# Optimization experiments

Measured on AMD Instinct MI355X. Metric: run time of the kernel, lower is better.

The kernel has to match this reference:

```python
import jax, jax.numpy as jnp
import numpy as np

MESH_RESOLUTION = 0.1
ORDER = 3  # TSC interpolation


def setup_inputs() -> dict:
    key = jax.random.key(0)
    k1, k2 = jax.random.split(key)
    L = 20.0
    N, C = 100000, 8
    positions = jax.random.uniform(k1, (N, 3), dtype=jnp.float32) * L
    cell = jnp.eye(3, dtype=jnp.float32) * L
    embeddings = jax.random.normal(k2, (N, C), dtype=jnp.float32)
    return {"positions": positions, "cell": cell, "embeddings": embeddings}


def _weights_order3(dist):
    # dist: [N,3]; returns [3,N,3]
    d2 = dist * dist
    return jnp.stack([
        0.125 * (1.0 - 4.0 * dist + 4.0 * d2),
        0.25 * (3.0 - 4.0 * d2),
        0.125 * (1.0 + 4.0 * dist + 4.0 * d2),
    ])


def reference(positions, cell, embeddings):
    # Mesh setup (cubic box)
    mesh_size = float(jnp.trace(cell)) / 3.0
    n_mesh = int(2 * round(mesh_size / (2.0 * MESH_RESOLUTION)))
    spacing = mesh_size / n_mesh
    C = embeddings.shape[1]

    positions_cell = positions / spacing  # [N,3]
    # odd order: nearest-grid-point centering
    idx = jnp.round(positions_cell).astype(jnp.int32)  # [N,3]
    dist = positions_cell - idx.astype(positions_cell.dtype)  # [N,3]

    w = _weights_order3(dist)  # [3,N,3]
    offs = jnp.arange(1 - (ORDER + 1) // 2, 1 + ORDER // 2)  # [-1,0,1]
    rp = (idx[None, :, :] + offs[:, None, None]) % n_mesh  # [3,N,3]

    xs, ys, zs = jnp.meshgrid(jnp.arange(ORDER), jnp.arange(ORDER), jnp.arange(ORDER), indexing='ij')
    xs, ys, zs = xs.ravel(), ys.ravel(), zs.ravel()  # [27]

    # flat grid indices and combined weights per (corner, atom)
    flat_idx = (rp[xs, :, 0] * n_mesh + rp[ys, :, 1]) * n_mesh + rp[zs, :, 2]  # [27,N]
    wprod = w[xs, :, 0] * w[ys, :, 1] * w[zs, :, 2]  # [27,N]

    vals = wprod[:, :, None] * embeddings[None, :, :]  # [27,N,C]
    grid = jnp.zeros((n_mesh ** 3, C), dtype=positions.dtype)
    grid = grid.at[flat_idx.reshape(-1)].add(vals.reshape(-1, C))
    # -> (C, n, n, n) to match mesh.values layout
    return grid.reshape(n_mesh, n_mesh, n_mesh, C).transpose(3, 0, 1, 2)
```

## Files before the change

### kernel.cpp

```cpp
#include <hip/hip_runtime.h>
#include <math.h>


#define KColCAP 16
#define TYS 2
#define BLK 128

typedef float nfloat4 __attribute__((ext_vector_type(4)));

__device__ __forceinline__ float tsc_w(int o, float d) {
    float t = 0.5f + (float)o * d;
    return (o == 0) ? (0.75f - d * d) : (0.5f * t * t);
}

__device__ __forceinline__ float inv_spacing(const float* __restrict__ cell, int n) {
    float tr = cell[0] + cell[4] + cell[8];
    return (3.0f * (float)n) / tr;
}


__global__ __launch_bounds__(256) void fill_recs(
    const float* __restrict__ pos, const float* __restrict__ cell,
    const float* __restrict__ emb,
    int* __restrict__ counts, int* __restrict__ ovf_cnt,
    float4* __restrict__ binrec, int* __restrict__ ovf,
    int N, int n)
{
    int i = blockIdx.x * blockDim.x + threadIdx.x;
    if (i >= N) return;
    float inv_sp = inv_spacing(cell, n);
    float px = pos[3 * i + 0] * inv_sp;
    float py = pos[3 * i + 1] * inv_sp;
    float pz = pos[3 * i + 2] * inv_sp;
    int cx = (int)rintf(px); if (cx >= n) cx -= n; else if (cx < 0) cx += n;
    int cy = (int)rintf(py); if (cy >= n) cy -= n; else if (cy < 0) cy += n;
    int bin = cx * n + cy;
    int slot = atomicAdd(&counts[bin], 1);
    if (slot < KColCAP) {
        const float4* e4 = (const float4*)(emb + (size_t)i * 8);
        float4* r = binrec + (size_t)(bin * KColCAP + slot) * 3;
        r[0] = make_float4(px, py, pz, 0.0f);
        r[1] = e4[0];
        r[2] = e4[1];
    } else {
        int o = atomicAdd(ovf_cnt, 1);
        ovf[o] = i;
    }
}


__global__ __launch_bounds__(BLK) void deposit_slab2(
    const float4* __restrict__ binrec, const int* __restrict__ counts,
    float* __restrict__ out, int n, int nyg)
{
    extern __shared__ float lds[];
    const int tid = threadIdx.x;
    const int b = blockIdx.x;
    const int x = b / nyg, yg = b - x * nyg;
    const int y0 = yg * TYS;
    const int plane = TYS * n;
    const int sz4 = (8 * plane) >> 2;

    for (int i = tid; i < sz4; i += BLK)
        ((float4*)lds)[i] = make_float4(0.f, 0.f, 0.f, 0.f);

    __shared__ int s_base[12], s_cnt[12], s_pref[13];
    if (tid < 12) {
        int dxb = tid / 4 - 1;
        int jy  = tid & 3;
        int xb = x + dxb; if (xb < 0) xb += n; else if (xb >= n) xb -= n;
        int yb = y0 - 1 + jy; if (yb < 0) yb += n; else if (yb >= n) yb -= n;
        int bin = xb * n + yb;
        s_base[tid] = bin * KColCAP;
        int c = counts[bin];
        s_cnt[tid] = (c < KColCAP) ? c : KColCAP;
    }
    __syncthreads();
    if (tid == 0) {
        int r = 0;
        #pragma unroll
        for (int j = 0; j < 12; ++j) { s_pref[j] = r; r += s_cnt[j]; }
        s_pref[12] = r;
    }
    __syncthreads();
    const int tot = s_pref[12];
    const int half = n >> 1;

    for (int v = tid; v < tot; v += BLK) {
        int j = 0;
        #pragma unroll
        for (int k = 1; k < 12; ++k) j += (v >= s_pref[k]);
        const float4* rp = binrec + (size_t)(s_base[j] + (v - s_pref[j])) * 3;
        float4 P  = rp[0];
        float4 e0 = rp[1];
        float4 e1 = rp[2];

        int cx = (int)rintf(P.x); float dx = P.x - (float)cx;
        int cy = (int)rintf(P.y); float dy = P.y - (float)cy;
        int cz = (int)rintf(P.z); float dz = P.z - (float)cz;
        if (cx >= n) cx -= n; else if (cx < 0) cx += n;
        if (cy >= n) cy -= n; else if (cy < 0) cy += n;
        if (cz >= n) cz -= n; else if (cz < 0) cz += n;

        int rx = cx - x;  if (rx > half) rx -= n; else if (rx < -half) rx += n;
        int ry = cy - y0; if (ry > half) ry -= n; else if (ry < -half) ry += n;

        float wx = tsc_w(-rx, dx);

        float wys[3] = { wx * tsc_w(-1, dy), wx * tsc_w(0, dy), wx * tsc_w(1, dy) };
        float wzs[3] = { tsc_w(-1, dz), tsc_w(0, dz), tsc_w(1, dz) };
        int lz0 = cz - 1; if (lz0 < 0) lz0 += n;
        int lz2 = cz + 1; if (lz2 >= n) lz2 -= n;
        int lzs[3] = { lz0, cz, lz2 };

        #pragma unroll
        for (int kb = 0; kb < 3; ++kb) {
            int ly = ry + kb - 1;
            if (ly < 0 || ly >= TYS) continue;
            float wvy = wys[kb];
            #pragma unroll
            for (int kc = 0; kc < 3; ++kc) {
                float w = wvy * wzs[kc];
                float* p = lds + ly * n + lzs[kc];
                atomicAdd(p + 0 * plane, w * e0.x);
                atomicAdd(p + 1 * plane, w * e0.y);
                atomicAdd(p + 2 * plane, w * e0.z);
                atomicAdd(p + 3 * plane, w * e0.w);
                atomicAdd(p + 4 * plane, w * e1.x);
                atomicAdd(p + 5 * plane, w * e1.y);
                atomicAdd(p + 6 * plane, w * e1.z);
                atomicAdd(p + 7 * plane, w * e1.w);
            }
        }
    }
    __syncthreads();

    const size_t n3 = (size_t)n * n * n;
    const int chunk = plane >> 2;
    #pragma unroll
    for (int ch = 0; ch < 8; ++ch) {
        const nfloat4* src = (const nfloat4*)(lds + (size_t)ch * plane);
        nfloat4* dst = (nfloat4*)(out + (size_t)ch * n3 + (size_t)x * n * n + (size_t)y0 * n);
        for (int i = tid; i < chunk; i += BLK)
            __builtin_nontemporal_store(src[i], dst + i);
    }
}

__global__ __launch_bounds__(256) void deposit_overflow(
    const float* __restrict__ pos, const float* __restrict__ cell,
    const float* __restrict__ emb, const int* __restrict__ ovf_cnt,
    const int* __restrict__ ovf, float* __restrict__ out, int n)
{
    int m = *ovf_cnt;
    int i = blockIdx.x * blockDim.x + threadIdx.x;
    if (i >= m) return;
    int ai = ovf[i];
    float inv_sp = inv_spacing(cell, n);
    float p[3], d[3]; int c0[3];
    #pragma unroll
    for (int kk = 0; kk < 3; ++kk) {
        p[kk] = pos[3 * ai + kk] * inv_sp;
        c0[kk] = (int)rintf(p[kk]);
        d[kk] = p[kk] - (float)c0[kk];
    }
    float w[3][3];
    #pragma unroll
    for (int kk = 0; kk < 3; ++kk) {
        float dd = d[kk];
        w[kk][0] = tsc_w(-1, dd); w[kk][1] = tsc_w(0, dd); w[kk][2] = tsc_w(1, dd);
    }
    int W[3][3];
    #pragma unroll
    for (int kk = 0; kk < 3; ++kk)
        #pragma unroll
        for (int a = 0; a < 3; ++a) {
            int v = c0[kk] - 1 + a; if (v < 0) v += n; else if (v >= n) v -= n;
            W[kk][a] = v;
        }
    size_t n3 = (size_t)n * n * n;
    const float4* e4 = (const float4*)(emb + (size_t)ai * 8);
    float4 e0 = e4[0], e1 = e4[1];
    float e[8] = {e0.x, e0.y, e0.z, e0.w, e1.x, e1.y, e1.z, e1.w};
    for (int a = 0; a < 3; ++a)
        for (int bq = 0; bq < 3; ++bq)
            for (int cq = 0; cq < 3; ++cq) {
                float wt = w[0][a] * w[1][bq] * w[2][cq];
                size_t g = ((size_t)W[0][a] * n + W[1][bq]) * n + W[2][cq];
                #pragma unroll
                for (int ch = 0; ch < 8; ++ch)
                    atomicAdd(out + (size_t)ch * n3 + g, wt * e[ch]);
            }
}


__global__ __launch_bounds__(256) void deposit_tsc8_ilv(
    const float* __restrict__ pos,
    const float* __restrict__ cell,
    const float* __restrict__ emb,
    float* __restrict__ ws,
    int total, int n)
{
    int t = blockIdx.x * blockDim.x + threadIdx.x;
    if (t >= total) return;
    int atom = t / 27;
    int c    = t - atom * 27;
    int a    = c / 9;
    int rem  = c - a * 9;
    int b    = rem / 3;
    int cc   = rem - b * 3;

    float inv_sp = inv_spacing(cell, n);

    float px = pos[3 * atom + 0] * inv_sp;
    float py = pos[3 * atom + 1] * inv_sp;
    float pz = pos[3 * atom + 2] * inv_sp;

    int cx = (int)rintf(px);  float dx = px - (float)cx;
    int cy = (int)rintf(py);  float dy = py - (float)cy;
    int cz = (int)rintf(pz);  float dz = pz - (float)cz;

    float w = tsc_w(a - 1, dx) * tsc_w(b - 1, dy) * tsc_w(cc - 1, dz);

    int x = cx - 1 + a;  if (x < 0) x += n; else if (x >= n) x -= n;
    int y = cy - 1 + b;  if (y < 0) y += n; else if (y >= n) y -= n;
    int z = cz - 1 + cc; if (z < 0) z += n; else if (z >= n) z -= n;

    const float4* e4 = (const float4*)(emb + (size_t)atom * 8);
    float4 e0 = e4[0], e1 = e4[1];

    float* p = ws + ((size_t)((x * n + y) * n + z)) * 8;
    atomicAdd(p + 0, w * e0.x);
    atomicAdd(p + 1, w * e0.y);
    atomicAdd(p + 2, w * e0.z);
    atomicAdd(p + 3, w * e0.w);
    atomicAdd(p + 4, w * e1.x);
    atomicAdd(p + 5, w * e1.y);
    atomicAdd(p + 6, w * e1.z);
    atomicAdd(p + 7, w * e1.w);
}

__global__ __launch_bounds__(256) void transpose_ilv8(
    const float* __restrict__ ws, float* __restrict__ out, int n3)
{
    int t = blockIdx.x * blockDim.x + threadIdx.x;
    int g0 = t * 4;
    if (g0 >= n3) return;
    const float4* w4 = (const float4*)(ws + (size_t)g0 * 8);
    float4 r0 = w4[0], r1 = w4[1];
    float4 r2 = w4[2], r3 = w4[3];
    float4 r4 = w4[4], r5 = w4[5];
    float4 r6 = w4[6], r7 = w4[7];

    *(float4*)(out + (size_t)0 * n3 + g0) = make_float4(r0.x, r2.x, r4.x, r6.x);
    *(float4*)(out + (size_t)1 * n3 + g0) = make_float4(r0.y, r2.y, r4.y, r6.y);
    *(float4*)(out + (size_t)2 * n3 + g0) = make_float4(r0.z, r2.z, r4.z, r6.z);
    *(float4*)(out + (size_t)3 * n3 + g0) = make_float4(r0.w, r2.w, r4.w, r6.w);
    *(float4*)(out + (size_t)4 * n3 + g0) = make_float4(r1.x, r3.x, r5.x, r7.x);
    *(float4*)(out + (size_t)5 * n3 + g0) = make_float4(r1.y, r3.y, r5.y, r7.y);
    *(float4*)(out + (size_t)6 * n3 + g0) = make_float4(r1.z, r3.z, r5.z, r7.z);
    *(float4*)(out + (size_t)7 * n3 + g0) = make_float4(r1.w, r3.w, r5.w, r7.w);
}


__global__ __launch_bounds__(256) void deposit_tsc_gen(
    const float* __restrict__ pos,
    const float* __restrict__ cell,
    const float* __restrict__ emb,
    float* __restrict__ out,
    int N, int n, int C)
{
    int i = blockIdx.x * blockDim.x + threadIdx.x;
    if (i >= N) return;

    float inv_sp = inv_spacing(cell, n);

    float p[3], d[3];
    int c0[3];
    #pragma unroll
    for (int k = 0; k < 3; ++k) {
        p[k] = pos[3 * i + k] * inv_sp;
        c0[k] = (int)rintf(p[k]);
        d[k] = p[k] - (float)c0[k];
    }
    float w[3][3];
    #pragma unroll
    for (int k = 0; k < 3; ++k) {
        float dd = d[k], d2 = dd * dd;
        w[k][0] = 0.125f * (1.0f - 4.0f * dd + 4.0f * d2);
        w[k][1] = 0.25f  * (3.0f - 4.0f * d2);
        w[k][2] = 0.125f * (1.0f + 4.0f * dd + 4.0f * d2);
    }
    int W[3][3];
    #pragma unroll
    for (int k = 0; k < 3; ++k) {
        #pragma unroll
        for (int a = 0; a < 3; ++a) {
            int v = c0[k] - 1 + a; if (v < 0) v += n; else if (v >= n) v -= n;
            W[k][a] = v;
        }
    }
    int n3 = n * n * n;
    for (int a = 0; a < 3; ++a)
        for (int b = 0; b < 3; ++b)
            for (int cc = 0; cc < 3; ++cc) {
                float wt = w[0][a] * w[1][b] * w[2][cc];
                int g = (W[0][a] * n + W[1][b]) * n + W[2][cc];
                for (int ch = 0; ch < C; ++ch)
                    atomicAdd(out + (size_t)ch * n3 + g, wt * emb[(size_t)i * C + ch]);
            }
}

extern "C" void kernel_launch(void* const* d_in, const int* in_sizes, int n_in,
                              void* d_out, int out_size, void* d_ws, size_t ws_size,
                              hipStream_t stream) {
    const float* pos  = (const float*)d_in[0];
    const float* cell = (const float*)d_in[1];
    const float* emb  = (const float*)d_in[2];
    float* out = (float*)d_out;
    float* ws  = (float*)d_ws;

    int N = in_sizes[0] / 3;
    int C = in_sizes[2] / N;
    long long n3l = (long long)out_size / C;
    int n = (int)llroundf(cbrtf((float)n3l));
    int n3 = (int)n3l;

    int block = 256;

    {
        int nb = n * n;
        size_t lds_bytes = (size_t)8 * TYS * n * sizeof(float);
        size_t rec_off = (((size_t)nb + 4 + (size_t)N) * sizeof(int) + 15) & ~(size_t)15;
        size_t need = rec_off + (size_t)nb * KColCAP * 48;
        bool slab_ok = (C == 8) && (n % TYS == 0) && n >= 8 && n <= 512
                       && lds_bytes <= 64 * 1024
                       && ws_size >= need
                       && ((long long)n * n * n == n3l);
        if (slab_ok) {
            int* counts  = (int*)d_ws;
            int* ovf_cnt = counts + nb;
            int* ovf     = counts + nb + 4;
            float4* binrec = (float4*)((char*)d_ws + rec_off);

            (void)hipMemsetAsync(counts, 0, (size_t)(nb + 4) * sizeof(int), stream);
            fill_recs<<<(N + block - 1) / block, block, 0, stream>>>(
                pos, cell, emb, counts, ovf_cnt, binrec, ovf, N, n);
            int nyg = n / TYS;
            deposit_slab2<<<n * nyg, BLK, lds_bytes, stream>>>(
                binrec, counts, out, n, nyg);
            deposit_overflow<<<(N + block - 1) / block, block, 0, stream>>>(
                pos, cell, emb, ovf_cnt, ovf, out, n);
            return;
        }
    }

    size_t need = (size_t)out_size * sizeof(float);
    if (C == 8 && ws_size >= need && (n3 % 4) == 0) {
        (void)hipMemsetAsync(d_ws, 0, need, stream);
        int total = N * 27;
        deposit_tsc8_ilv<<<(total + block - 1) / block, block, 0, stream>>>(
            pos, cell, emb, ws, total, n);
        int tthreads = n3 / 4;
        transpose_ilv8<<<(tthreads + block - 1) / block, block, 0, stream>>>(
            ws, out, n3);
    } else {
        (void)hipMemsetAsync(d_out, 0, (size_t)out_size * sizeof(float), stream);
        int grid = (N + block - 1) / block;
        deposit_tsc_gen<<<grid, block, 0, stream>>>(pos, cell, emb, out, N, n, C);
    }
}
```

Measured before the change: 157.9 us.

## Convert slab deposit kernel into persistent blocks looping over contiguous tiles

Replaces the one-block-per-(x, y-pair) slab deposit launch with a persistent kernel of about 2048 blocks. Each block processes a contiguous range of tiles, zeroing LDS, gathering and accumulating bin records, then streaming the tile out with a flattened channel-major store loop. The aim is to cut block launch and scheduling overhead across the 20000 small tiles and to improve locality in the per-block bin reads. In exchange each block now runs its tiles serially with an extra barrier per tile, and load balance can get worse. The slab path's size limit also tightens to n at most 256.

```diff
diff --git a/kernel.cpp b/kernel.cpp
--- a/kernel.cpp
+++ b/kernel.cpp
@@ -5,6 +5,7 @@
 #define KColCAP 16
 #define TYS 2
 #define BLK 128
+#define BPCU 8
 
 typedef float nfloat4 __attribute__((ext_vector_type(4)));
 
@@ -49,100 +50,108 @@
 }
 
 
-__global__ __launch_bounds__(BLK) void deposit_slab2(
+__global__ __launch_bounds__(BLK) void deposit_persist(
     const float4* __restrict__ binrec, const int* __restrict__ counts,
-    float* __restrict__ out, int n, int nyg)
+    float* __restrict__ out, int n, int nyg, int ntiles, int tpb)
 {
     extern __shared__ float lds[];
     const int tid = threadIdx.x;
-    const int b = blockIdx.x;
-    const int x = b / nyg, yg = b - x * nyg;
-    const int y0 = yg * TYS;
     const int plane = TYS * n;
-    const int sz4 = (8 * plane) >> 2;
-
-    for (int i = tid; i < sz4; i += BLK)
-        ((float4*)lds)[i] = make_float4(0.f, 0.f, 0.f, 0.f);
+    const int q4 = plane >> 2;
+    const int nf4 = 8 * q4;
+    const int half = n >> 1;
+    const size_t n3 = (size_t)n * n * n;
 
     __shared__ int s_base[12], s_cnt[12], s_pref[13];
-    if (tid < 12) {
-        int dxb = tid / 4 - 1;
-        int jy  = tid & 3;
-        int xb = x + dxb; if (xb < 0) xb += n; else if (xb >= n) xb -= n;
-        int yb = y0 - 1 + jy; if (yb < 0) yb += n; else if (yb >= n) yb -= n;
-        int bin = xb * n + yb;
-        s_base[tid] = bin * KColCAP;
-        int c = counts[bin];
-        s_cnt[tid] = (c < KColCAP) ? c : KColCAP;
-    }
-    __syncthreads();
-    if (tid == 0) {
-        int r = 0;
-        #pragma unroll
-        for (int j = 0; j < 12; ++j) { s_pref[j] = r; r += s_cnt[j]; }
-        s_pref[12] = r;
-    }
-    __syncthreads();
-    const int tot = s_pref[12];
-    const int half = n >> 1;
-
-    for (int v = tid; v < tot; v += BLK) {
-        int j = 0;
-        #pragma unroll
-        for (int k = 1; k < 12; ++k) j += (v >= s_pref[k]);
-        const float4* rp = binrec + (size_t)(s_base[j] + (v - s_pref[j])) * 3;
-        float4 P  = rp[0];
-        float4 e0 = rp[1];
-        float4 e1 = rp[2];
-
-        int cx = (int)rintf(P.x); float dx = P.x - (float)cx;
-        int cy = (int)rintf(P.y); float dy = P.y - (float)cy;
-        int cz = (int)rintf(P.z); float dz = P.z - (float)cz;
-        if (cx >= n) cx -= n; else if (cx < 0) cx += n;
-        if (cy >= n) cy -= n; else if (cy < 0) cy += n;
-        if (cz >= n) cz -= n; else if (cz < 0) cz += n;
-
-        int rx = cx - x;  if (rx > half) rx -= n; else if (rx < -half) rx += n;
-        int ry = cy - y0; if (ry > half) ry -= n; else if (ry < -half) ry += n;
-
-        float wx = tsc_w(-rx, dx);
-
-        float wys[3] = { wx * tsc_w(-1, dy), wx * tsc_w(0, dy), wx * tsc_w(1, dy) };
-        float wzs[3] = { tsc_w(-1, dz), tsc_w(0, dz), tsc_w(1, dz) };
-        int lz0 = cz - 1; if (lz0 < 0) lz0 += n;
-        int lz2 = cz + 1; if (lz2 >= n) lz2 -= n;
-        int lzs[3] = { lz0, cz, lz2 };
-
-        #pragma unroll
-        for (int kb = 0; kb < 3; ++kb) {
-            int ly = ry + kb - 1;
-            if (ly < 0 || ly >= TYS) continue;
-            float wvy = wys[kb];
+
+    int t0 = blockIdx.x * tpb;
+    int t1 = t0 + tpb; if (t1 > ntiles) t1 = ntiles;
+
+    for (int t = t0; t < t1; ++t) {
+        const int x = t / nyg, yg = t - x * nyg;
+        const int y0 = yg * TYS;
+
+        for (int i = tid; i < nf4; i += BLK)
+            ((nfloat4*)lds)[i] = (nfloat4)(0.f);
+
+        if (tid < 12) {
+            int dxb = tid / 4 - 1;
+            int jy  = tid & 3;
+            int xb = x + dxb; if (xb < 0) xb += n; else if (xb >= n) xb -= n;
+            int yb = y0 - 1 + jy; if (yb < 0) yb += n; else if (yb >= n) yb -= n;
+            int bin = xb * n + yb;
+            s_base[tid] = bin * KColCAP;
+            int c = counts[bin];
+            s_cnt[tid] = (c < KColCAP) ? c : KColCAP;
+        }
+        __syncthreads();
+        if (tid == 0) {
+            int r = 0;
             #pragma unroll
-            for (int kc = 0; kc < 3; ++kc) {
-                float w = wvy * wzs[kc];
-                float* p = lds + ly * n + lzs[kc];
-                atomicAdd(p + 0 * plane, w * e0.x);
-                atomicAdd(p + 1 * plane, w * e0.y);
-                atomicAdd(p + 2 * plane, w * e0.z);
-                atomicAdd(p + 3 * plane, w * e0.w);
-                atomicAdd(p + 4 * plane, w * e1.x);
-                atomicAdd(p + 5 * plane, w * e1.y);
-                atomicAdd(p + 6 * plane, w * e1.z);
-                atomicAdd(p + 7 * plane, w * e1.w);
+            for (int j = 0; j < 12; ++j) { s_pref[j] = r; r += s_cnt[j]; }
+            s_pref[12] = r;
+        }
+        __syncthreads();
+        const int tot = s_pref[12];
+
+        for (int v = tid; v < tot; v += BLK) {
+            int j = 0;
+            #pragma unroll
+            for (int k = 1; k < 12; ++k) j += (v >= s_pref[k]);
+            const float4* rp = binrec + (size_t)(s_base[j] + (v - s_pref[j])) * 3;
+            float4 P  = rp[0];
+            float4 e0 = rp[1];
+            float4 e1 = rp[2];
+
+            int cx = (int)rintf(P.x); float dx = P.x - (float)cx;
+            int cy = (int)rintf(P.y); float dy = P.y - (float)cy;
+            int cz = (int)rintf(P.z); float dz = P.z - (float)cz;
+            if (cx >= n) cx -= n; else if (cx < 0) cx += n;
+            if (cy >= n) cy -= n; else if (cy < 0) cy += n;
+            if (cz >= n) cz -= n; else if (cz < 0) cz += n;
+
+            int rx = cx - x;  if (rx > half) rx -= n; else if (rx < -half) rx += n;
+            int ry = cy - y0; if (ry > half) ry -= n; else if (ry < -half) ry += n;
+
+            float wx = tsc_w(-rx, dx);
+
+            float wys[3] = { wx * tsc_w(-1, dy), wx * tsc_w(0, dy), wx * tsc_w(1, dy) };
+            float wzs[3] = { tsc_w(-1, dz), tsc_w(0, dz), tsc_w(1, dz) };
+            int lz0 = cz - 1; if (lz0 < 0) lz0 += n;
+            int lz2 = cz + 1; if (lz2 >= n) lz2 -= n;
+            int lzs[3] = { lz0, cz, lz2 };
+
+            #pragma unroll
+            for (int kb = 0; kb < 3; ++kb) {
+                int ly = ry + kb - 1;
+                if (ly < 0 || ly >= TYS) continue;
+                float wvy = wys[kb];
+                #pragma unroll
+                for (int kc = 0; kc < 3; ++kc) {
+                    float w = wvy * wzs[kc];
+                    float* p = lds + ly * n + lzs[kc];
+                    atomicAdd(p + 0 * plane, w * e0.x);
+                    atomicAdd(p + 1 * plane, w * e0.y);
+                    atomicAdd(p + 2 * plane, w * e0.z);
+                    atomicAdd(p + 3 * plane, w * e0.w);
+                    atomicAdd(p + 4 * plane, w * e1.x);
+                    atomicAdd(p + 5 * plane, w * e1.y);
+                    atomicAdd(p + 6 * plane, w * e1.z);
+                    atomicAdd(p + 7 * plane, w * e1.w);
+                }
             }
         }
-    }
-    __syncthreads();
-
-    const size_t n3 = (size_t)n * n * n;
-    const int chunk = plane >> 2;
-    #pragma unroll
-    for (int ch = 0; ch < 8; ++ch) {
-        const nfloat4* src = (const nfloat4*)(lds + (size_t)ch * plane);
-        nfloat4* dst = (nfloat4*)(out + (size_t)ch * n3 + (size_t)x * n * n + (size_t)y0 * n);
-        for (int i = tid; i < chunk; i += BLK)
-            __builtin_nontemporal_store(src[i], dst + i);
+        __syncthreads();
+
+        float* outb = out + (size_t)x * n * n + (size_t)y0 * n;
+        for (int i = tid; i < nf4; i += BLK) {
+            int ch = i / q4;
+            int q  = i - ch * q4;
+            nfloat4 v = ((const nfloat4*)lds)[i];
+            __builtin_nontemporal_store(
+                v, (nfloat4*)(outb + (size_t)ch * n3) + q);
+        }
+        __syncthreads();
     }
 }
 
@@ -332,7 +341,7 @@
         size_t lds_bytes = (size_t)8 * TYS * n * sizeof(float);
         size_t rec_off = (((size_t)nb + 4 + (size_t)N) * sizeof(int) + 15) & ~(size_t)15;
         size_t need = rec_off + (size_t)nb * KColCAP * 48;
-        bool slab_ok = (C == 8) && (n % TYS == 0) && n >= 8 && n <= 512
+        bool slab_ok = (C == 8) && (n % TYS == 0) && n >= 8 && n <= 256
                        && lds_bytes <= 64 * 1024
                        && ws_size >= need
                        && ((long long)n * n * n == n3l);
@@ -345,9 +354,15 @@
             (void)hipMemsetAsync(counts, 0, (size_t)(nb + 4) * sizeof(int), stream);
             fill_recs<<<(N + block - 1) / block, block, 0, stream>>>(
                 pos, cell, emb, counts, ovf_cnt, binrec, ovf, N, n);
+
             int nyg = n / TYS;
-            deposit_slab2<<<n * nyg, BLK, lds_bytes, stream>>>(
-                binrec, counts, out, n, nyg);
+            int ntiles = n * nyg;
+            int nblocks = 256 * BPCU;
+            if (nblocks > ntiles) nblocks = ntiles;
+            int tpb = (ntiles + nblocks - 1) / nblocks;
+            deposit_persist<<<nblocks, BLK, lds_bytes, stream>>>(
+                binrec, counts, out, n, nyg, ntiles, tpb);
+
             deposit_overflow<<<(N + block - 1) / block, block, 0, stream>>>(
                 pos, cell, emb, ovf_cnt, ovf, out, n);
             return;
```

New measurement: 179.2 us. 1.13x slower.

## Persistent producer-consumer deposit kernel with double-buffered LDS slabs

Applied to the files above, without the earlier changes.

Replaces the one-block-per-tile slab deposit with a persistent kernel over a fixed grid of blocks. In each block, half the threads scatter particles into one LDS buffer with atomics while the other half stream the previous tile's buffer to global memory. The aim is to overlap the global writeback with the LDS accumulation and to amortise block launch and zeroing. It also pads the channel stride, uses a custom LDS barrier, and computes the prefix sums in registers. In exchange, only 128 threads accumulate per tile, LDS use doubles, and the path is now limited to n <= 256.

```diff
diff --git a/kernel.cpp b/kernel.cpp
--- a/kernel.cpp
+++ b/kernel.cpp
@@ -4,9 +4,17 @@
 
 #define KColCAP 16
 #define TYS 2
-#define BLK 128
+#define BLK 256
+#define NBLK 1536
 
 typedef float nfloat4 __attribute__((ext_vector_type(4)));
+
+__device__ __forceinline__ void block_sync_lds() {
+    __builtin_amdgcn_sched_barrier(0);
+    asm volatile("s_waitcnt lgkmcnt(0)" ::: "memory");
+    __builtin_amdgcn_s_barrier();
+    __builtin_amdgcn_sched_barrier(0);
+}
 
 __device__ __forceinline__ float tsc_w(int o, float d) {
     float t = 0.5f + (float)o * d;
@@ -49,100 +57,138 @@
 }
 
 
-__global__ __launch_bounds__(BLK) void deposit_slab2(
+__global__ __launch_bounds__(BLK) void deposit_pc(
     const float4* __restrict__ binrec, const int* __restrict__ counts,
-    float* __restrict__ out, int n, int nyg)
+    float* __restrict__ out, int n, int nyg, int ntiles)
 {
     extern __shared__ float lds[];
     const int tid = threadIdx.x;
-    const int b = blockIdx.x;
-    const int x = b / nyg, yg = b - x * nyg;
-    const int y0 = yg * TYS;
+    const int bid = blockIdx.x;
+    const int grid = gridDim.x;
     const int plane = TYS * n;
-    const int sz4 = (8 * plane) >> 2;
-
-    for (int i = tid; i < sz4; i += BLK)
-        ((float4*)lds)[i] = make_float4(0.f, 0.f, 0.f, 0.f);
-
-    __shared__ int s_base[12], s_cnt[12], s_pref[13];
-    if (tid < 12) {
-        int dxb = tid / 4 - 1;
-        int jy  = tid & 3;
-        int xb = x + dxb; if (xb < 0) xb += n; else if (xb >= n) xb -= n;
-        int yb = y0 - 1 + jy; if (yb < 0) yb += n; else if (yb >= n) yb -= n;
-        int bin = xb * n + yb;
-        s_base[tid] = bin * KColCAP;
-        int c = counts[bin];
-        s_cnt[tid] = (c < KColCAP) ? c : KColCAP;
-    }
-    __syncthreads();
-    if (tid == 0) {
-        int r = 0;
+    const int cstr = plane + 4;
+    const int bufsz = 8 * cstr;
+    const int q4 = plane >> 2;
+    const int half = n >> 1;
+    const size_t n3 = (size_t)n * n * n;
+    const bool producer = (tid < 128);
+    const int ctid = tid - 128;
+
+    int iter = 0;
+    int pt = -1;
+
+    for (int t = bid; t < ntiles; t += grid, ++iter) {
+        const int p = iter & 1;
+        float* bufp = lds + p * bufsz;
+
+        if (producer) {
+            nfloat4* z4 = (nfloat4*)bufp;
+            const int nz4 = bufsz >> 2;
+            for (int i = tid; i < nz4; i += 128)
+                z4[i] = (nfloat4)(0.f);
+        } else if (iter > 0) {
+            const float* src = lds + (p ^ 1) * bufsz;
+            const int px_ = pt / nyg, pyg = pt - px_ * nyg;
+            const int py0 = pyg * TYS;
+            float* outb = out + (size_t)px_ * n * n + (size_t)py0 * n;
+            #pragma unroll
+            for (int ch = 0; ch < 8; ++ch) {
+                const nfloat4* s4 = (const nfloat4*)(src + ch * cstr);
+                nfloat4* d4 = (nfloat4*)(outb + (size_t)ch * n3);
+                for (int q = ctid; q < q4; q += 128)
+                    __builtin_nontemporal_store(s4[q], d4 + q);
+            }
+        }
+        block_sync_lds();
+
+        if (producer) {
+            const int x = t / nyg, yg = t - x * nyg;
+            const int y0 = yg * TYS;
+
+            int base[12], pref[13];
+            pref[0] = 0;
+            #pragma unroll
+            for (int j = 0; j < 12; ++j) {
+                int dxb = j >> 2;
+                int jy  = j & 3;
+                int xb = x + dxb - 1; if (xb < 0) xb += n; else if (xb >= n) xb -= n;
+                int yb = y0 - 1 + jy; if (yb < 0) yb += n; else if (yb >= n) yb -= n;
+                int bin = xb * n + yb;
+                base[j] = bin * KColCAP;
+                int c = counts[bin];
+                c = (c < KColCAP) ? c : KColCAP;
+                pref[j + 1] = pref[j] + c;
+            }
+            const int tot = pref[12];
+
+            for (int v = tid; v < tot; v += 128) {
+                int rec = base[0] + v;
+                #pragma unroll
+                for (int k = 1; k < 12; ++k) {
+                    int cand = base[k] + (v - pref[k]);
+                    rec = (v >= pref[k]) ? cand : rec;
+                }
+                const float4* rp = binrec + (size_t)rec * 3;
+                float4 P  = rp[0];
+                float4 e0 = rp[1];
+                float4 e1 = rp[2];
+
+                int cx = (int)rintf(P.x); float dx = P.x - (float)cx;
+                int cy = (int)rintf(P.y); float dy = P.y - (float)cy;
+                int cz = (int)rintf(P.z); float dz = P.z - (float)cz;
+                if (cx >= n) cx -= n; else if (cx < 0) cx += n;
+                if (cy >= n) cy -= n; else if (cy < 0) cy += n;
+                if (cz >= n) cz -= n; else if (cz < 0) cz += n;
+
+                int rx = cx - x;  if (rx > half) rx -= n; else if (rx < -half) rx += n;
+                int ry = cy - y0; if (ry > half) ry -= n; else if (ry < -half) ry += n;
+
+                float wx = tsc_w(-rx, dx);
+
+                float wys[3] = { wx * tsc_w(-1, dy), wx * tsc_w(0, dy), wx * tsc_w(1, dy) };
+                float wzs[3] = { tsc_w(-1, dz), tsc_w(0, dz), tsc_w(1, dz) };
+                int lz0 = cz - 1; if (lz0 < 0) lz0 += n;
+                int lz2 = cz + 1; if (lz2 >= n) lz2 -= n;
+                int lzs[3] = { lz0, cz, lz2 };
+
+                #pragma unroll
+                for (int kb = 0; kb < 3; ++kb) {
+                    int ly = ry + kb - 1;
+                    if (ly < 0 || ly >= TYS) continue;
+                    float wvy = wys[kb];
+                    #pragma unroll
+                    for (int kc = 0; kc < 3; ++kc) {
+                        float w = wvy * wzs[kc];
+                        float* q = bufp + ly * n + lzs[kc];
+                        atomicAdd(q + 0 * cstr, w * e0.x);
+                        atomicAdd(q + 1 * cstr, w * e0.y);
+                        atomicAdd(q + 2 * cstr, w * e0.z);
+                        atomicAdd(q + 3 * cstr, w * e0.w);
+                        atomicAdd(q + 4 * cstr, w * e1.x);
+                        atomicAdd(q + 5 * cstr, w * e1.y);
+                        atomicAdd(q + 6 * cstr, w * e1.z);
+                        atomicAdd(q + 7 * cstr, w * e1.w);
+                    }
+                }
+            }
+        }
+        block_sync_lds();
+        pt = t;
+    }
+
+    if (!producer && iter > 0) {
+        const int p = (iter - 1) & 1;
+        const float* src = lds + p * bufsz;
+        const int px_ = pt / nyg, pyg = pt - px_ * nyg;
+        const int py0 = pyg * TYS;
+        float* outb = out + (size_t)px_ * n * n + (size_t)py0 * n;
         #pragma unroll
-        for (int j = 0; j < 12; ++j) { s_pref[j] = r; r += s_cnt[j]; }
-        s_pref[12] = r;
-    }
-    __syncthreads();
-    const int tot = s_pref[12];
-    const int half = n >> 1;
-
-    for (int v = tid; v < tot; v += BLK) {
-        int j = 0;
-        #pragma unroll
-        for (int k = 1; k < 12; ++k) j += (v >= s_pref[k]);
-        const float4* rp = binrec + (size_t)(s_base[j] + (v - s_pref[j])) * 3;
-        float4 P  = rp[0];
-        float4 e0 = rp[1];
-        float4 e1 = rp[2];
-
-        int cx = (int)rintf(P.x); float dx = P.x - (float)cx;
-        int cy = (int)rintf(P.y); float dy = P.y - (float)cy;
-        int cz = (int)rintf(P.z); float dz = P.z - (float)cz;
-        if (cx >= n) cx -= n; else if (cx < 0) cx += n;
-        if (cy >= n) cy -= n; else if (cy < 0) cy += n;
-        if (cz >= n) cz -= n; else if (cz < 0) cz += n;
-
-        int rx = cx - x;  if (rx > half) rx -= n; else if (rx < -half) rx += n;
-        int ry = cy - y0; if (ry > half) ry -= n; else if (ry < -half) ry += n;
-
-        float wx = tsc_w(-rx, dx);
-
-        float wys[3] = { wx * tsc_w(-1, dy), wx * tsc_w(0, dy), wx * tsc_w(1, dy) };
-        float wzs[3] = { tsc_w(-1, dz), tsc_w(0, dz), tsc_w(1, dz) };
-        int lz0 = cz - 1; if (lz0 < 0) lz0 += n;
-        int lz2 = cz + 1; if (lz2 >= n) lz2 -= n;
-        int lzs[3] = { lz0, cz, lz2 };
-
-        #pragma unroll
-        for (int kb = 0; kb < 3; ++kb) {
-            int ly = ry + kb - 1;
-            if (ly < 0 || ly >= TYS) continue;
-            float wvy = wys[kb];
-            #pragma unroll
-            for (int kc = 0; kc < 3; ++kc) {
-                float w = wvy * wzs[kc];
-                float* p = lds + ly * n + lzs[kc];
-                atomicAdd(p + 0 * plane, w * e0.x);
-                atomicAdd(p + 1 * plane, w * e0.y);
-                atomicAdd(p + 2 * plane, w * e0.z);
-                atomicAdd(p + 3 * plane, w * e0.w);
-                atomicAdd(p + 4 * plane, w * e1.x);
-                atomicAdd(p + 5 * plane, w * e1.y);
-                atomicAdd(p + 6 * plane, w * e1.z);
-                atomicAdd(p + 7 * plane, w * e1.w);
-            }
-        }
-    }
-    __syncthreads();
-
-    const size_t n3 = (size_t)n * n * n;
-    const int chunk = plane >> 2;
-    #pragma unroll
-    for (int ch = 0; ch < 8; ++ch) {
-        const nfloat4* src = (const nfloat4*)(lds + (size_t)ch * plane);
-        nfloat4* dst = (nfloat4*)(out + (size_t)ch * n3 + (size_t)x * n * n + (size_t)y0 * n);
-        for (int i = tid; i < chunk; i += BLK)
-            __builtin_nontemporal_store(src[i], dst + i);
+        for (int ch = 0; ch < 8; ++ch) {
+            const nfloat4* s4 = (const nfloat4*)(src + ch * cstr);
+            nfloat4* d4 = (nfloat4*)(outb + (size_t)ch * n3);
+            for (int q = ctid; q < q4; q += 128)
+                __builtin_nontemporal_store(s4[q], d4 + q);
+        }
     }
 }
 
@@ -329,14 +375,14 @@
 
     {
         int nb = n * n;
-        size_t lds_bytes = (size_t)8 * TYS * n * sizeof(float);
+        size_t lds_bytes = (size_t)2 * 8 * (TYS * n + 4) * sizeof(float);
         size_t rec_off = (((size_t)nb + 4 + (size_t)N) * sizeof(int) + 15) & ~(size_t)15;
         size_t need = rec_off + (size_t)nb * KColCAP * 48;
-        bool slab_ok = (C == 8) && (n % TYS == 0) && n >= 8 && n <= 512
-                       && lds_bytes <= 64 * 1024
-                       && ws_size >= need
-                       && ((long long)n * n * n == n3l);
-        if (slab_ok) {
+        bool ok = (C == 8) && (n % TYS == 0) && (n % 4 == 0) && n >= 8 && n <= 256
+                  && lds_bytes <= 64 * 1024
+                  && ws_size >= need
+                  && ((long long)n * n * n == n3l);
+        if (ok) {
             int* counts  = (int*)d_ws;
             int* ovf_cnt = counts + nb;
             int* ovf     = counts + nb + 4;
@@ -345,9 +391,14 @@
             (void)hipMemsetAsync(counts, 0, (size_t)(nb + 4) * sizeof(int), stream);
             fill_recs<<<(N + block - 1) / block, block, 0, stream>>>(
                 pos, cell, emb, counts, ovf_cnt, binrec, ovf, N, n);
+
             int nyg = n / TYS;
-            deposit_slab2<<<n * nyg, BLK, lds_bytes, stream>>>(
-                binrec, counts, out, n, nyg);
+            int ntiles = n * nyg;
+            int nblocks = NBLK;
+            if (nblocks > ntiles) nblocks = ntiles;
+            deposit_pc<<<nblocks, BLK, lds_bytes, stream>>>(
+                binrec, counts, out, n, nyg, ntiles);
+
             deposit_overflow<<<(N + block - 1) / block, block, 0, stream>>>(
                 pos, cell, emb, ovf_cnt, ovf, out, n);
             return;
```

New measurement: 162.4 us. +2.9%, slower.

## Replace LDS atomic scatter slab deposit with per-column register gather kernel

Applied to the files above, without the earlier changes.

The slab kernel scattered each atom's 27 weighted contributions into shared memory with atomics and then copied the slab out. It is replaced by a gather kernel in which each thread owns four consecutive z cells of one (x,y) column. That thread loops over the atoms in the 9 neighbouring xy bins, builds TSC weights on the fly and accumulates all 8 channels in registers. This drops the LDS zeroing, the atomics and the barriers, and each thread writes its results with coalesced vector stores. The cost is redundant weight math across lanes that read the same atoms, and idle lanes when n/4 is below 64.

```diff
diff --git a/kernel.cpp b/kernel.cpp
--- a/kernel.cpp
+++ b/kernel.cpp
@@ -3,8 +3,6 @@
 
 
 #define KColCAP 16
-#define TYS 2
-#define BLK 128
 
 typedef float nfloat4 __attribute__((ext_vector_type(4)));
 
@@ -49,100 +47,86 @@
 }
 
 
-__global__ __launch_bounds__(BLK) void deposit_slab2(
+__global__ __launch_bounds__(256) void gather_col(
     const float4* __restrict__ binrec, const int* __restrict__ counts,
-    float* __restrict__ out, int n, int nyg)
-{
-    extern __shared__ float lds[];
-    const int tid = threadIdx.x;
-    const int b = blockIdx.x;
-    const int x = b / nyg, yg = b - x * nyg;
-    const int y0 = yg * TYS;
-    const int plane = TYS * n;
-    const int sz4 = (8 * plane) >> 2;
-
-    for (int i = tid; i < sz4; i += BLK)
-        ((float4*)lds)[i] = make_float4(0.f, 0.f, 0.f, 0.f);
-
-    __shared__ int s_base[12], s_cnt[12], s_pref[13];
-    if (tid < 12) {
-        int dxb = tid / 4 - 1;
-        int jy  = tid & 3;
-        int xb = x + dxb; if (xb < 0) xb += n; else if (xb >= n) xb -= n;
-        int yb = y0 - 1 + jy; if (yb < 0) yb += n; else if (yb >= n) yb -= n;
-        int bin = xb * n + yb;
-        s_base[tid] = bin * KColCAP;
-        int c = counts[bin];
-        s_cnt[tid] = (c < KColCAP) ? c : KColCAP;
-    }
-    __syncthreads();
-    if (tid == 0) {
-        int r = 0;
-        #pragma unroll
-        for (int j = 0; j < 12; ++j) { s_pref[j] = r; r += s_cnt[j]; }
-        s_pref[12] = r;
-    }
-    __syncthreads();
-    const int tot = s_pref[12];
+    float* __restrict__ out, int n, int nzc)
+{
+    const int lane = threadIdx.x & 63;
+    const int y = blockIdx.x * 4 + (threadIdx.x >> 6);
+    const int x = blockIdx.y;
+    if (lane >= nzc) return;
+    const int z0 = lane * 4;
     const int half = n >> 1;
 
-    for (int v = tid; v < tot; v += BLK) {
-        int j = 0;
-        #pragma unroll
-        for (int k = 1; k < 12; ++k) j += (v >= s_pref[k]);
-        const float4* rp = binrec + (size_t)(s_base[j] + (v - s_pref[j])) * 3;
-        float4 P  = rp[0];
-        float4 e0 = rp[1];
-        float4 e1 = rp[2];
-
-        int cx = (int)rintf(P.x); float dx = P.x - (float)cx;
-        int cy = (int)rintf(P.y); float dy = P.y - (float)cy;
-        int cz = (int)rintf(P.z); float dz = P.z - (float)cz;
-        if (cx >= n) cx -= n; else if (cx < 0) cx += n;
-        if (cy >= n) cy -= n; else if (cy < 0) cy += n;
-        if (cz >= n) cz -= n; else if (cz < 0) cz += n;
-
-        int rx = cx - x;  if (rx > half) rx -= n; else if (rx < -half) rx += n;
-        int ry = cy - y0; if (ry > half) ry -= n; else if (ry < -half) ry += n;
-
-        float wx = tsc_w(-rx, dx);
-
-        float wys[3] = { wx * tsc_w(-1, dy), wx * tsc_w(0, dy), wx * tsc_w(1, dy) };
-        float wzs[3] = { tsc_w(-1, dz), tsc_w(0, dz), tsc_w(1, dz) };
-        int lz0 = cz - 1; if (lz0 < 0) lz0 += n;
-        int lz2 = cz + 1; if (lz2 >= n) lz2 -= n;
-        int lzs[3] = { lz0, cz, lz2 };
-
-        #pragma unroll
-        for (int kb = 0; kb < 3; ++kb) {
-            int ly = ry + kb - 1;
-            if (ly < 0 || ly >= TYS) continue;
-            float wvy = wys[kb];
-            #pragma unroll
-            for (int kc = 0; kc < 3; ++kc) {
-                float w = wvy * wzs[kc];
-                float* p = lds + ly * n + lzs[kc];
-                atomicAdd(p + 0 * plane, w * e0.x);
-                atomicAdd(p + 1 * plane, w * e0.y);
-                atomicAdd(p + 2 * plane, w * e0.z);
-                atomicAdd(p + 3 * plane, w * e0.w);
-                atomicAdd(p + 4 * plane, w * e1.x);
-                atomicAdd(p + 5 * plane, w * e1.y);
-                atomicAdd(p + 6 * plane, w * e1.z);
-                atomicAdd(p + 7 * plane, w * e1.w);
+    int cnt[3][3], cb[3][3];
+    #pragma unroll
+    for (int jx = 0; jx < 3; ++jx) {
+        int xb = x + jx - 1; if (xb < 0) xb += n; else if (xb >= n) xb -= n;
+        #pragma unroll
+        for (int jy = 0; jy < 3; ++jy) {
+            int yb = y + jy - 1; if (yb < 0) yb += n; else if (yb >= n) yb -= n;
+            int bin = xb * n + yb;
+            cb[jx][jy] = bin * KColCAP;
+            int c = counts[bin];
+            cnt[jx][jy] = (c < KColCAP) ? c : KColCAP;
+        }
+    }
+
+    float acc[4][8];
+    #pragma unroll
+    for (int zk = 0; zk < 4; ++zk)
+        #pragma unroll
+        for (int ch = 0; ch < 8; ++ch) acc[zk][ch] = 0.0f;
+
+    #pragma unroll
+    for (int jx = 0; jx < 3; ++jx) {
+        #pragma unroll
+        for (int jy = 0; jy < 3; ++jy) {
+            const int c = cnt[jx][jy];
+            const float4* rb = binrec + (size_t)cb[jx][jy] * 3;
+            for (int s = 0; s < c; ++s) {
+                float4 P  = rb[3 * s + 0];
+                float4 e0 = rb[3 * s + 1];
+                float4 e1 = rb[3 * s + 2];
+
+                float cxf = rintf(P.x); float dx = P.x - cxf;
+                float cyf = rintf(P.y); float dy = P.y - cyf;
+                float czf = rintf(P.z); float dz = P.z - czf;
+                int cz = (int)czf; if (cz >= n) cz -= n; else if (cz < 0) cz += n;
+
+                float tx = 0.5f + (float)(1 - jx) * dx;
+                float wx = (jx == 1) ? (0.75f - dx * dx) : (0.5f * tx * tx);
+                float ty = 0.5f + (float)(1 - jy) * dy;
+                float wy = (jy == 1) ? (0.75f - dy * dy) : (0.5f * ty * ty);
+                float wxy = wx * wy;
+
+                #pragma unroll
+                for (int zk = 0; zk < 4; ++zk) {
+                    int dzi = z0 + zk - cz;
+                    if (dzi > half) dzi -= n; else if (dzi < -half) dzi += n;
+                    float fd = (float)dzi;
+                    float t = 0.5f + fd * dz;
+                    float wz = (dzi == 0) ? (0.75f - dz * dz) : (0.5f * t * t);
+                    float w = (fabsf(fd) <= 1.0f) ? wxy * wz : 0.0f;
+                    acc[zk][0] += w * e0.x;
+                    acc[zk][1] += w * e0.y;
+                    acc[zk][2] += w * e0.z;
+                    acc[zk][3] += w * e0.w;
+                    acc[zk][4] += w * e1.x;
+                    acc[zk][5] += w * e1.y;
+                    acc[zk][6] += w * e1.z;
+                    acc[zk][7] += w * e1.w;
+                }
             }
         }
     }
-    __syncthreads();
 
     const size_t n3 = (size_t)n * n * n;
-    const int chunk = plane >> 2;
+    const size_t colbase = ((size_t)x * n + y) * (size_t)n + z0;
     #pragma unroll
     for (int ch = 0; ch < 8; ++ch) {
-        const nfloat4* src = (const nfloat4*)(lds + (size_t)ch * plane);
-        nfloat4* dst = (nfloat4*)(out + (size_t)ch * n3 + (size_t)x * n * n + (size_t)y0 * n);
-        for (int i = tid; i < chunk; i += BLK)
-            __builtin_nontemporal_store(src[i], dst + i);
+        nfloat4 v = { acc[0][ch], acc[1][ch], acc[2][ch], acc[3][ch] };
+        __builtin_nontemporal_store(v, (nfloat4*)(out + (size_t)ch * n3 + colbase));
     }
 }
 
@@ -329,14 +313,12 @@
 
     {
         int nb = n * n;
-        size_t lds_bytes = (size_t)8 * TYS * n * sizeof(float);
         size_t rec_off = (((size_t)nb + 4 + (size_t)N) * sizeof(int) + 15) & ~(size_t)15;
         size_t need = rec_off + (size_t)nb * KColCAP * 48;
-        bool slab_ok = (C == 8) && (n % TYS == 0) && n >= 8 && n <= 512
-                       && lds_bytes <= 64 * 1024
-                       && ws_size >= need
-                       && ((long long)n * n * n == n3l);
-        if (slab_ok) {
+        bool ok = (C == 8) && (n % 4 == 0) && n >= 8 && n <= 256
+                  && ws_size >= need
+                  && ((long long)n * n * n == n3l);
+        if (ok) {
             int* counts  = (int*)d_ws;
             int* ovf_cnt = counts + nb;
             int* ovf     = counts + nb + 4;
@@ -345,9 +327,11 @@
             (void)hipMemsetAsync(counts, 0, (size_t)(nb + 4) * sizeof(int), stream);
             fill_recs<<<(N + block - 1) / block, block, 0, stream>>>(
                 pos, cell, emb, counts, ovf_cnt, binrec, ovf, N, n);
-            int nyg = n / TYS;
-            deposit_slab2<<<n * nyg, BLK, lds_bytes, stream>>>(
-                binrec, counts, out, n, nyg);
+
+            dim3 grid(n / 4, n);
+            gather_col<<<grid, block, 0, stream>>>(
+                binrec, counts, out, n, n / 4);
+
             deposit_overflow<<<(N + block - 1) / block, block, 0, stream>>>(
                 pos, cell, emb, ovf_cnt, ovf, out, n);
             return;
```

Result: slower. 170.7 us (+8.1%).
